# Performance work log

Hardware: AMD Instinct MI355X
Metric: run time of the kernel (lower is better)

Reference implementation:

```python
import jax, jax.numpy as jnp
import numpy as np
from jax import lax

WS = 8      # window size (square)
SS = 4      # shift size
HEADS = 8
K = 9       # snake-conv kernel size
CENTER = K // 2
EXT = 1.0   # extend_scope


def _shift_attn_mask(H, W):
    # static numpy construction of Swin shift mask -> [num_windows, L, L]
    m = np.zeros((H, W), dtype=np.float32)
    cnt = 0
    for hs in [(0, -WS), (-WS, -SS), (-SS, None)]:
        for ws_ in [(0, -WS), (-WS, -SS), (-SS, None)]:
            m[hs[0]:hs[1], ws_[0]:ws_[1]] = cnt
            cnt += 1
    m = m.reshape(H // WS, WS, W // WS, WS).transpose(0, 2, 1, 3).reshape(-1, WS * WS)
    d = m[:, None, :] - m[:, :, None]
    return jnp.asarray(np.where(d != 0, -100.0, 0.0).astype(np.float32))


def shifted_window_attention(x, qkv_w, qkv_b, proj_w, proj_b, rel_bias):
    B, H, W, C = x.shape
    d = C // HEADS
    x = jnp.roll(x, shift=(-SS, -SS), axis=(1, 2))
    nH, nW = H // WS, W // WS
    nwin, L = nH * nW, WS * WS
    # window partition -> [B*nwin, L, C]
    xw = x.reshape(B, nH, WS, nW, WS, C).transpose(0, 1, 3, 2, 4, 5).reshape(B * nwin, L, C)
    qkv = (xw @ qkv_w.T + qkv_b).reshape(B * nwin, L, 3, HEADS, d).transpose(2, 0, 3, 1, 4)
    q, k, v = qkv[0] * (d ** -0.5), qkv[1], qkv[2]
    attn = jnp.einsum('nhld,nhmd->nhlm', q, k) + rel_bias[None]
    amask = _shift_attn_mask(H, W)  # [nwin, L, L]
    attn = attn.reshape(B, nwin, HEADS, L, L) + amask[None, :, None]
    attn = jax.nn.softmax(attn.reshape(B * nwin, HEADS, L, L), axis=-1)
    out = jnp.einsum('nhlm,nhmd->nhld', attn, v).transpose(0, 2, 1, 3).reshape(B * nwin, L, C)
    out = out @ proj_w.T + proj_b
    out = out.reshape(B, nH, nW, WS, WS, C).transpose(0, 1, 3, 2, 4, 5).reshape(B, H, W, C)
    return jnp.roll(out, shift=(SS, SS), axis=(1, 2))


def snake_coordinate_map(offset):
    # offset [B, 2K, Wd, Hd], morph=0: cumulative y offsets from the kernel center
    B, _, Wd, Hd = offset.shape
    y_off = offset[:, :K]
    # y_new[center]=0; y_new[center+i]=sum_{j=1..i} y_off[center+j]; mirror below
    up = jnp.cumsum(y_off[:, CENTER + 1:], axis=1)
    down = jnp.cumsum(y_off[:, :CENTER][:, ::-1], axis=1)[:, ::-1]
    y_cum = jnp.concatenate([down, jnp.zeros((B, 1, Wd, Hd), offset.dtype), up], axis=1)
    y_center = jnp.arange(Wd, dtype=offset.dtype)[None, None, :, None]
    y_new = y_center + EXT * y_cum                              # [B,K,Wd,Hd]
    x_spread = jnp.linspace(-CENTER, CENTER, K, dtype=offset.dtype)[None, :, None, None]
    x_center = jnp.arange(Hd, dtype=offset.dtype)[None, None, None, :]
    x_new = jnp.broadcast_to(x_center + x_spread, (B, K, Wd, Hd))
    # rearrange 'b k w h -> b (w k) h'
    y_map = y_new.transpose(0, 2, 1, 3).reshape(B, Wd * K, Hd)
    x_map = x_new.transpose(0, 2, 1, 3).reshape(B, Wd * K, Hd)
    return y_map, x_map


def bilinear_sample(feat, ymap, xmap):
    Hin, Win = feat.shape[-2], feat.shape[-1]
    y = jnp.clip(ymap, 0.0, Hin - 1.0)
    x = jnp.clip(xmap, 0.0, Win - 1.0)
    y0f, x0f = jnp.floor(y), jnp.floor(x)
    wy, wx = y - y0f, x - x0f
    y0 = y0f.astype(jnp.int32); x0 = x0f.astype(jnp.int32)
    y1 = jnp.minimum(y0 + 1, Hin - 1); x1 = jnp.minimum(x0 + 1, Win - 1)
    g = jax.vmap(lambda f, yy, xx: f[:, yy, xx])  # -> [B,C,Ho,Wo]
    v00 = g(feat, y0, x0); v01 = g(feat, y0, x1)
    v10 = g(feat, y1, x0); v11 = g(feat, y1, x1)
    wy = wy[:, None]; wx = wx[:, None]
    return v00 * (1 - wy) * (1 - wx) + v01 * (1 - wy) * wx + v10 * wy * (1 - wx) + v11 * wy * wx


def _forward(x, qkv_weight, qkv_bias, proj_weight, proj_bias, rel_bias, offset, dsc_weight, dsc_bias):
    y = shifted_window_attention(x, qkv_weight, qkv_bias, proj_weight, proj_bias, rel_bias)
    feat = y.transpose(0, 3, 1, 2)                      # NCHW
    ymap, xmap = snake_coordinate_map(offset)
    samp = bilinear_sample(feat, ymap, xmap)            # [B,C,H*K,W]
    out = lax.conv_general_dilated(samp, dsc_weight, window_strides=(K, 1), padding='VALID',
                                   dimension_numbers=('NCHW', 'OIHW', 'NCHW'))
    return jax.nn.relu(out + dsc_bias[None, :, None, None])


def setup_inputs() -> dict:
    key = jax.random.key(0)
    ks = jax.random.split(key, 9)
    B, H, W, C = 8, 64, 64, 256
    return {
        'x': jax.random.normal(ks[0], (B, H, W, C), jnp.float32),
        'qkv_weight': jax.random.normal(ks[1], (3 * C, C), jnp.float32) * 0.05,
        'qkv_bias': jax.random.normal(ks[2], (3 * C,), jnp.float32) * 0.05,
        'proj_weight': jax.random.normal(ks[3], (C, C), jnp.float32) * 0.05,
        'proj_bias': jax.random.normal(ks[4], (C,), jnp.float32) * 0.05,
        'rel_bias': jax.random.normal(ks[5], (HEADS, WS * WS, WS * WS), jnp.float32) * 0.05,
        'offset': jax.random.normal(ks[6], (B, 2 * K, H, W), jnp.float32),
        'dsc_weight': jax.random.normal(ks[7], (C, C, K, 1), jnp.float32) * 0.02,
        'dsc_bias': jax.random.normal(ks[8], (C,), jnp.float32) * 0.02,
    }


def reference(x, qkv_weight, qkv_bias, proj_weight, proj_bias, rel_bias, offset, dsc_weight, dsc_bias):
    return _forward(x, qkv_weight, qkv_bias, proj_weight, proj_bias, rel_bias, offset, dsc_weight, dsc_bias)
```

## Files before the change

### kernel.cpp

```cpp
#include <hip/hip_runtime.h>
#include <math.h>


#define NFLOAT_BUF 8388608

typedef float f32x4 __attribute__((ext_vector_type(4)));
typedef __bf16 bf16x8 __attribute__((ext_vector_type(8)));
typedef _Float16 f16x8 __attribute__((ext_vector_type(8)));

__device__ inline unsigned pack2_bf16(float a, float b) {
    union { float f; unsigned u; } ua, ub;
    ua.f = a; ub.f = b;
    unsigned ra = (ua.u + 0x7FFFu + ((ua.u >> 16) & 1u)) >> 16;
    unsigned rb = (ub.u + 0x7FFFu + ((ub.u >> 16) & 1u)) & 0xFFFF0000u;
    return (ra & 0xFFFFu) | rb;
}

__global__ __launch_bounds__(256) void prep_kernel(
    const float* __restrict__ x, unsigned short* __restrict__ xb,
    const float* __restrict__ qkv_w, unsigned short* __restrict__ wb,
    const float* __restrict__ proj_w, _Float16* __restrict__ pwh,
    const float* __restrict__ dsc_w, _Float16* __restrict__ wT,
    const float* __restrict__ offset, float* __restrict__ ymap) {
    int bid = blockIdx.x, tid = threadIdx.x;
    if (bid < 4096) {
        int t = bid * 256 + tid;
        const float4* s = (const float4*)(x + (size_t)t * 8);
        float4 a = s[0], b = s[1];
        uint4 o;
        o.x = pack2_bf16(a.x, a.y); o.y = pack2_bf16(a.z, a.w);
        o.z = pack2_bf16(b.x, b.y); o.w = pack2_bf16(b.z, b.w);
        *(uint4*)(xb + (size_t)t * 8) = o;
    } else if (bid < 4192) {
        int t = (bid - 4096) * 256 + tid;
        if (t < 24576) {
            const float4* s = (const float4*)(qkv_w + (size_t)t * 8);
            float4 a = s[0], b = s[1];
            uint4 o;
            o.x = pack2_bf16(a.x, a.y); o.y = pack2_bf16(a.z, a.w);
            o.z = pack2_bf16(b.x, b.y); o.w = pack2_bf16(b.z, b.w);
            *(uint4*)(wb + (size_t)t * 8) = o;
        }
    } else if (bid < 4224) {
        int t = (bid - 4192) * 256 + tid;
        if (t < 8192) {
            const float4* s = (const float4*)(proj_w + (size_t)t * 8);
            float4 a = s[0], b = s[1];
            union { _Float16 h[8]; uint4 u; } o;
            o.h[0] = (_Float16)a.x; o.h[1] = (_Float16)a.y;
            o.h[2] = (_Float16)a.z; o.h[3] = (_Float16)a.w;
            o.h[4] = (_Float16)b.x; o.h[5] = (_Float16)b.y;
            o.h[6] = (_Float16)b.z; o.h[7] = (_Float16)b.w;
            *(uint4*)(pwh + (size_t)t * 8) = o.u;
        }
    } else if (bid < 6528) {
        int t = (bid - 4224) * 256 + tid;
        int o = t / 2304;
        int kk = t - o * 2304;
        int k = kk >> 8, i = kk & 255;
        wT[t] = (_Float16)dsc_w[(o * 256 + i) * 9 + k];
    } else {
        int t = (bid - 6528) * 256 + tid;
        int hd = t & 63;
        int wd = (t >> 6) & 63;
        int b  = t >> 12;
        const float* op = offset + ((size_t)(b * 18) * 64 + wd) * 64 + hd;
        float yo[9];
        #pragma unroll
        for (int k = 0; k < 9; ++k) yo[k] = op[(size_t)k * 4096];
        float cum[9];
        cum[4] = 0.0f;
        float s = 0.0f;
        for (int j = 3; j >= 0; --j) { s += yo[j]; cum[j] = s; }
        s = 0.0f;
        for (int j = 5; j < 9; ++j) { s += yo[j]; cum[j] = s; }
        float wdf = (float)wd;
        float* yp = ymap + ((size_t)(b * 576 + wd * 9)) * 64 + hd;
        #pragma unroll
        for (int k = 0; k < 9; ++k) yp[(size_t)k * 64] = wdf + cum[k];
    }
}

__global__ __launch_bounds__(256) void qkv_mfma_kernel(
    const unsigned short* __restrict__ xb, const unsigned short* __restrict__ wb,
    const float* __restrict__ qkv_b,
    _Float16* __restrict__ qh, _Float16* __restrict__ kh, _Float16* __restrict__ vt) {

    __shared__ __align__(16) char Asb[8192];
    __shared__ __align__(16) char Bsb[32768];
    __shared__ unsigned rowoff[64];

    int nb = blockIdx.x;
    int m0 = blockIdx.y * 64;
    int tid = threadIdx.x;
    int lane = tid & 63, w = tid >> 6;
    int gw = m0 >> 6;

    if (tid < 64) {
        int l = tid;
        int b = gw >> 6, win = gw & 63;
        int rh = ((win >> 3) << 3) + (l >> 3);
        int rw = ((win & 7) << 3) + (l & 7);
        int sh = (rh + 4) & 63, sw = (rw + 4) & 63;
        rowoff[l] = (unsigned)(((b * 64 + sh) * 64 + sw) * 512);
    }

    f32x4 acc[4][4];
    #pragma unroll
    for (int m = 0; m < 4; ++m)
        #pragma unroll
        for (int n = 0; n < 4; ++n) {
            f32x4 z = {0.0f, 0.0f, 0.0f, 0.0f};
            acc[m][n] = z;
        }

    const char* xc = (const char*)xb;
    const char* wc = (const char*)wb;
    int rA = (lane & 15) * 128;
    int u0 = (((lane >> 4)    ) ^ (lane & 7)) << 4;
    int u1 = ((4 + (lane >> 4)) ^ (lane & 7)) << 4;

    __syncthreads();

    for (int c = 0; c < 4; ++c) {
        #pragma unroll
        for (int r = 0; r < 2; ++r) {
            int pos = r * 256 + tid;
            int row = pos >> 3, u = pos & 7;
            const char* src = xc + rowoff[row] + c * 128 + ((u ^ (row & 7)) << 4);
            __builtin_amdgcn_global_load_lds(
                (const __attribute__((address_space(1))) unsigned int*)src,
                (__attribute__((address_space(3))) unsigned int*)(Asb + pos * 16),
                16, 0, 0);
        }
        #pragma unroll
        for (int r = 0; r < 8; ++r) {
            int pos = r * 256 + tid;
            int n = pos >> 3, u = pos & 7;
            const char* src = wc + (size_t)(nb * 256 + n) * 512 + c * 128 + ((u ^ (n & 7)) << 4);
            __builtin_amdgcn_global_load_lds(
                (const __attribute__((address_space(1))) unsigned int*)src,
                (__attribute__((address_space(3))) unsigned int*)(Bsb + pos * 16),
                16, 0, 0);
        }
        __syncthreads();

        bf16x8 av[4][2], bv[4][2];
        #pragma unroll
        for (int m = 0; m < 4; ++m) {
            av[m][0] = *(const bf16x8*)(Asb + m * 2048 + rA + u0);
            av[m][1] = *(const bf16x8*)(Asb + m * 2048 + rA + u1);
        }
        #pragma unroll
        for (int n = 0; n < 4; ++n) {
            bv[n][0] = *(const bf16x8*)(Bsb + w * 8192 + n * 2048 + rA + u0);
            bv[n][1] = *(const bf16x8*)(Bsb + w * 8192 + n * 2048 + rA + u1);
        }
        #pragma unroll
        for (int m = 0; m < 4; ++m)
            #pragma unroll
            for (int n = 0; n < 4; ++n) {
                acc[m][n] = __builtin_amdgcn_mfma_f32_16x16x32_bf16(av[m][0], bv[n][0], acc[m][n], 0, 0, 0);
                acc[m][n] = __builtin_amdgcn_mfma_f32_16x16x32_bf16(av[m][1], bv[n][1], acc[m][n], 0, 0, 0);
            }
        __syncthreads();
    }

    float scale = (nb == 0) ? 0.17677669529663689f : 1.0f;
    #pragma unroll
    for (int nf = 0; nf < 4; ++nf) {
        int o = w * 64 + nf * 16 + (lane & 15);
        float bias = qkv_b[nb * 256 + o];
        int hh = o >> 5, dd = o & 31;
        if (nb < 2) {
            _Float16* dstb = (nb == 0) ? qh : kh;
            _Float16* base = dstb + ((size_t)(gw * 8 + hh) * 64) * 32 + dd;
            #pragma unroll
            for (int mf = 0; mf < 4; ++mf) {
                int l0 = mf * 16 + (lane >> 4) * 4;
                #pragma unroll
                for (int j = 0; j < 4; ++j)
                    base[(size_t)(l0 + j) * 32] = (_Float16)((acc[mf][nf][j] + bias) * scale);
            }
        } else {
            _Float16* base = vt + ((size_t)(gw * 8 + hh) * 32 + dd) * 64;
            #pragma unroll
            for (int mf = 0; mf < 4; ++mf) {
                int l0 = mf * 16 + (lane >> 4) * 4;
                union { _Float16 x[4]; uint2 u; } pk;
                #pragma unroll
                for (int j = 0; j < 4; ++j) pk.x[j] = (_Float16)(acc[mf][nf][j] + bias);
                *(uint2*)(base + l0) = pk.u;
            }
        }
    }
}

__global__ __launch_bounds__(512, 4) void attn_proj_kernel(
    const _Float16* __restrict__ qh, const _Float16* __restrict__ kh,
    const _Float16* __restrict__ vt, const float* __restrict__ rel_bias,
    const _Float16* __restrict__ pwh, const float* __restrict__ proj_b,
    _Float16* __restrict__ feath) {

    __shared__ __align__(16) char SH[65536];
    int n = blockIdx.x;
    int win = n & 63;
    int wy = win >> 3, wx = win & 7;
    int tid = threadIdx.x, lane = tid & 63, h = tid >> 6;
    int qc = lane & 15, g = lane >> 4;
    char* P = SH + h * 8192;

    const _Float16* qp = qh + (size_t)(n * 8 + h) * 2048;
    const _Float16* kp = kh + (size_t)(n * 8 + h) * 2048;
    const _Float16* vp = vt + (size_t)(n * 8 + h) * 2048;
    const float* rb = rel_bias + (size_t)h * 4096;

    int rk[16];
    #pragma unroll
    for (int mt = 0; mt < 4; ++mt)
        #pragma unroll
        for (int j = 0; j < 4; ++j) {
            int key = mt * 16 + g * 4 + j;
            int rh = wy * 8 + (key >> 3), rw = wx * 8 + (key & 7);
            rk[mt * 4 + j] = (rh < 56 ? 0 : (rh < 60 ? 1 : 2)) * 3
                           + (rw < 56 ? 0 : (rw < 60 ? 1 : 2));
        }

    f16x8 kf[4];
    #pragma unroll
    for (int mt = 0; mt < 4; ++mt)
        kf[mt] = *(const f16x8*)(kp + (mt * 16 + qc) * 32 + g * 8);

    #pragma unroll
    for (int nt = 0; nt < 4; ++nt) {
        int q = nt * 16 + qc;
        int rqh = wy * 8 + (q >> 3), rqw = wx * 8 + (q & 7);
        int rq = (rqh < 56 ? 0 : (rqh < 60 ? 1 : 2)) * 3
               + (rqw < 56 ? 0 : (rqw < 60 ? 1 : 2));
        f16x8 qf = *(const f16x8*)(qp + q * 32 + g * 8);

        f32x4 s[4];
        #pragma unroll
        for (int mt = 0; mt < 4; ++mt) {
            f32x4 z = {0.0f, 0.0f, 0.0f, 0.0f};
            s[mt] = __builtin_amdgcn_mfma_f32_16x16x32_f16(kf[mt], qf, z, 0, 0, 0);
        }

        float vals[16];
        #pragma unroll
        for (int mt = 0; mt < 4; ++mt) {
            float4 bv4 = *(const float4*)(rb + q * 64 + mt * 16 + g * 4);
            vals[mt * 4 + 0] = s[mt][0] + bv4.x + (rk[mt * 4 + 0] != rq ? -100.0f : 0.0f);
            vals[mt * 4 + 1] = s[mt][1] + bv4.y + (rk[mt * 4 + 1] != rq ? -100.0f : 0.0f);
            vals[mt * 4 + 2] = s[mt][2] + bv4.z + (rk[mt * 4 + 2] != rq ? -100.0f : 0.0f);
            vals[mt * 4 + 3] = s[mt][3] + bv4.w + (rk[mt * 4 + 3] != rq ? -100.0f : 0.0f);
        }

        float mx = vals[0];
        #pragma unroll
        for (int i = 1; i < 16; ++i) mx = fmaxf(mx, vals[i]);
        mx = fmaxf(mx, __shfl_xor(mx, 16));
        mx = fmaxf(mx, __shfl_xor(mx, 32));

        float sum = 0.0f;
        #pragma unroll
        for (int i = 0; i < 16; ++i) { vals[i] = __expf(vals[i] - mx); sum += vals[i]; }
        sum += __shfl_xor(sum, 16);
        sum += __shfl_xor(sum, 32);
        float inv = 1.0f / sum;

        #pragma unroll
        for (int mt = 0; mt < 4; ++mt) {
            union { _Float16 x[4]; uint2 u; } pk4;
            #pragma unroll
            for (int j = 0; j < 4; ++j) pk4.x[j] = (_Float16)(vals[mt * 4 + j] * inv);
            int off = (mt * 32 + g * 8) ^ ((q & 7) << 4);
            *(uint2*)(P + q * 128 + off) = pk4.u;
        }
    }

    f16x8 pa[4][2];
    #pragma unroll
    for (int im = 0; im < 4; ++im)
        #pragma unroll
        for (int ks = 0; ks < 2; ++ks) {
            int row = im * 16 + qc;
            int off = (ks * 64 + g * 16) ^ ((row & 7) << 4);
            pa[im][ks] = *(const f16x8*)(P + row * 128 + off);
        }
    f16x8 bvv[2][2];
    #pragma unroll
    for (int in = 0; in < 2; ++in)
        #pragma unroll
        for (int ks = 0; ks < 2; ++ks)
            bvv[in][ks] = *(const f16x8*)(vp + (in * 16 + qc) * 64 + ks * 32 + g * 8);

    f32x4 acc[4][2];
    #pragma unroll
    for (int im = 0; im < 4; ++im)
        #pragma unroll
        for (int in = 0; in < 2; ++in) {
            f32x4 z = {0.0f, 0.0f, 0.0f, 0.0f};
            acc[im][in] = z;
        }
    #pragma unroll
    for (int im = 0; im < 4; ++im)
        #pragma unroll
        for (int in = 0; in < 2; ++in) {
            acc[im][in] = __builtin_amdgcn_mfma_f32_16x16x32_f16(pa[im][0], bvv[in][0], acc[im][in], 0, 0, 0);
            acc[im][in] = __builtin_amdgcn_mfma_f32_16x16x32_f16(pa[im][1], bvv[in][1], acc[im][in], 0, 0, 0);
        }

    __syncthreads();

    char* aob = SH;
    char* Bsb = SH + 32768;
    #pragma unroll
    for (int im = 0; im < 4; ++im)
        #pragma unroll
        for (int in = 0; in < 2; ++in)
            #pragma unroll
            for (int j = 0; j < 4; ++j) {
                int row = im * 16 + g * 4 + j;
                int f = h * 32 + in * 16 + qc;
                *(_Float16*)(aob + row * 512 + ((((f >> 3) ^ (row & 7)) << 4) + (f & 7) * 2)) =
                    (_Float16)acc[im][in][j];
            }
    __syncthreads();

    int w04 = h & 3, wm = h >> 2;
    const char* wcp = (const char*)pwh;
    int bidx = n >> 6;

    f32x4 pacc[2][4];
    #pragma unroll
    for (int m = 0; m < 2; ++m)
        #pragma unroll
        for (int nn = 0; nn < 4; ++nn) {
            f32x4 z = {0.0f, 0.0f, 0.0f, 0.0f};
            pacc[m][nn] = z;
        }

    for (int c = 0; c < 4; ++c) {
        #pragma unroll
        for (int r = 0; r < 4; ++r) {
            int pos = r * 512 + tid;
            int nr = pos >> 3, uu = pos & 7;
            const char* src = wcp + (size_t)nr * 512 + c * 128 + ((uu ^ (nr & 7)) << 4);
            __builtin_amdgcn_global_load_lds(
                (const __attribute__((address_space(1))) unsigned int*)src,
                (__attribute__((address_space(3))) unsigned int*)(Bsb + pos * 16),
                16, 0, 0);
        }
        __syncthreads();

        f16x8 av2[2][2], bv2[4][2];
        #pragma unroll
        for (int m = 0; m < 2; ++m) {
            int row = wm * 32 + m * 16 + qc;
            #pragma unroll
            for (int ks = 0; ks < 2; ++ks) {
                int u = c * 8 + ks * 4 + g;
                av2[m][ks] = *(const f16x8*)(aob + row * 512 + ((u ^ (row & 7)) << 4));
            }
        }
        #pragma unroll
        for (int nn = 0; nn < 4; ++nn) {
            int oc = w04 * 64 + nn * 16 + qc;
            #pragma unroll
            for (int ks = 0; ks < 2; ++ks)
                bv2[nn][ks] = *(const f16x8*)(Bsb + oc * 128 + (((ks * 4 + g) ^ (oc & 7)) << 4));
        }
        #pragma unroll
        for (int m = 0; m < 2; ++m)
            #pragma unroll
            for (int nn = 0; nn < 4; ++nn) {
                pacc[m][nn] = __builtin_amdgcn_mfma_f32_16x16x32_f16(av2[m][0], bv2[nn][0], pacc[m][nn], 0, 0, 0);
                pacc[m][nn] = __builtin_amdgcn_mfma_f32_16x16x32_f16(av2[m][1], bv2[nn][1], pacc[m][nn], 0, 0, 0);
            }
        __syncthreads();
    }

    #pragma unroll
    for (int nn = 0; nn < 4; ++nn) {
        int f = w04 * 64 + nn * 16 + qc;
        float bias = proj_b[f];
        #pragma unroll
        for (int m = 0; m < 2; ++m) {
            #pragma unroll
            for (int j = 0; j < 4; ++j) {
                int px = wm * 32 + m * 16 + g * 4 + j;
                int rh = ((win >> 3) << 3) + (px >> 3);
                int rw = ((win & 7) << 3) + (px & 7);
                int p = (rh + 4) & 63;
                int qq = (rw + 4) & 63;
                feath[((size_t)(bidx * 64 + p) * 64 + qq) * 256 + f] =
                    (_Float16)(pacc[m][nn][j] + bias);
            }
        }
    }
}

__global__ __launch_bounds__(512) void sample_conv_mfma4_kernel(
    const _Float16* __restrict__ feath, const float* __restrict__ ymap,
    const _Float16* __restrict__ wT2h, const float* __restrict__ dsc_b,
    float* __restrict__ out) {

    __shared__ __align__(16) char Ab[2][16384];
    __shared__ __align__(16) char Bb[2][32768];
    __shared__ unsigned row0[2][9][64];
    __shared__ unsigned row1[2][9][64];
    __shared__ float    wyv[2][9][64];

    int blk = blockIdx.x;
    int b = blk & 7, wd0 = (blk >> 3) * 2;
    int tid = threadIdx.x;
    int lane = tid & 63, w = tid >> 6;
    int qc = lane & 15, g = lane >> 4;
    int ph = w >> 2, nq = w & 3;

    for (int idx = tid; idx < 1152; idx += 512) {
        int wdl = idx / 576;
        int r = idx - wdl * 576;
        int k = r >> 6, hd = r & 63;
        int wd = wd0 + wdl;
        float y = ymap[((size_t)(b * 576 + wd * 9 + k)) * 64 + hd];
        y = fminf(fmaxf(y, 0.0f), 63.0f);
        float y0f = floorf(y);
        int y0 = (int)y0f;
        int y1 = min(y0 + 1, 63);
        int xc = min(max(hd + k - 4, 0), 63);
        row0[wdl][k][hd] = (unsigned)(((b * 64 + y0) * 64 + xc) * 512);
        row1[wdl][k][hd] = (unsigned)(((b * 64 + y1) * 64 + xc) * 512);
        wyv[wdl][k][hd] = y - y0f;
    }

    f32x4 acc[4][4];
    #pragma unroll
    for (int m = 0; m < 4; ++m)
        #pragma unroll
        for (int n = 0; n < 4; ++n) {
            f32x4 z = {0.0f, 0.0f, 0.0f, 0.0f};
            acc[m][n] = z;
        }

    const char* featc = (const char*)feath;
    const char* wc    = (const char*)wT2h;

    int pxA[2], sAv[2];
    #pragma unroll
    for (int r = 0; r < 2; ++r) {
        int pos = r * 512 + tid;
        pxA[r] = pos >> 3;
        sAv[r] = pos & 7;
    }

    int rAa = qc * 128;
    int u0 = ((g    ) ^ (qc & 7)) << 4;
    int u1 = ((4 + g) ^ (qc & 7)) << 4;

    __syncthreads();

    #pragma unroll
    for (int r = 0; r < 4; ++r) {
        int pos = r * 512 + tid;
        int n = pos >> 3, uu = pos & 7;
        const char* src = wc + n * 4608 + 0 * 128 + ((uu ^ (n & 7)) << 4);
        __builtin_amdgcn_global_load_lds(
            (const __attribute__((address_space(1))) unsigned int*)src,
            (__attribute__((address_space(3))) unsigned int*)(Bb[0] + pos * 16),
            16, 0, 0);
    }
    #pragma unroll
    for (int r = 0; r < 2; ++r) {
        int px = pxA[r], sA = sAv[r];
        int wdl = px >> 6, hd = px & 63;
        unsigned b0 = row0[wdl][0][hd] + sA * 16;
        unsigned b1 = row1[wdl][0][hd] + sA * 16;
        float wy = wyv[wdl][0][hd];
        f16x8 v0 = *(const f16x8*)(featc + b0);
        f16x8 v1 = *(const f16x8*)(featc + b1);
        _Float16 wyh = (_Float16)wy;
        _Float16 omh = (_Float16)(1.0f - wy);
        f16x8 res = v0 * omh + v1 * wyh;
        *(f16x8*)(Ab[0] + px * 128 + ((sA ^ (px & 7)) << 4)) = res;
    }
    __syncthreads();

    for (int c = 0; c < 36; ++c) {
        int cur = c & 1, nxt = cur ^ 1;

        f16x8 s0[2], s1[2];
        float swy[2];
        if (c < 35) {
            int cn = c + 1;
            int ks = cn >> 2, cib = (cn & 3) * 128;
            #pragma unroll
            for (int r = 0; r < 4; ++r) {
                int pos = r * 512 + tid;
                int n = pos >> 3, uu = pos & 7;
                const char* src = wc + n * 4608 + cn * 128 + ((uu ^ (n & 7)) << 4);
                __builtin_amdgcn_global_load_lds(
                    (const __attribute__((address_space(1))) unsigned int*)src,
                    (__attribute__((address_space(3))) unsigned int*)(Bb[nxt] + pos * 16),
                    16, 0, 0);
            }
            #pragma unroll
            for (int r = 0; r < 2; ++r) {
                int px = pxA[r], sA = sAv[r];
                int wdl = px >> 6, hd = px & 63;
                unsigned b0 = row0[wdl][ks][hd] + cib + sA * 16;
                unsigned b1 = row1[wdl][ks][hd] + cib + sA * 16;
                swy[r] = wyv[wdl][ks][hd];
                s0[r] = *(const f16x8*)(featc + b0);
                s1[r] = *(const f16x8*)(featc + b1);
            }
        }

        f16x8 av[4][2], bv[4][2];
        #pragma unroll
        for (int m = 0; m < 4; ++m) {
            char* abase = Ab[cur] + ph * 8192 + m * 2048 + rAa;
            av[m][0] = *(const f16x8*)(abase + u0);
            av[m][1] = *(const f16x8*)(abase + u1);
        }
        #pragma unroll
        for (int n = 0; n < 4; ++n) {
            char* bbase = Bb[cur] + nq * 8192 + n * 2048 + rAa;
            bv[n][0] = *(const f16x8*)(bbase + u0);
            bv[n][1] = *(const f16x8*)(bbase + u1);
        }
        #pragma unroll
        for (int m = 0; m < 4; ++m)
            #pragma unroll
            for (int n = 0; n < 4; ++n) {
                acc[m][n] = __builtin_amdgcn_mfma_f32_16x16x32_f16(av[m][0], bv[n][0], acc[m][n], 0, 0, 0);
                acc[m][n] = __builtin_amdgcn_mfma_f32_16x16x32_f16(av[m][1], bv[n][1], acc[m][n], 0, 0, 0);
            }

        if (c < 35) {
            #pragma unroll
            for (int r = 0; r < 2; ++r) {
                int px = pxA[r], sA = sAv[r];
                _Float16 wyh = (_Float16)swy[r];
                _Float16 omh = (_Float16)(1.0f - swy[r]);
                f16x8 res = s0[r] * omh + s1[r] * wyh;
                *(f16x8*)(Ab[nxt] + px * 128 + ((sA ^ (px & 7)) << 4)) = res;
            }
        }
        __syncthreads();
    }

    #pragma unroll
    for (int n = 0; n < 4; ++n) {
        int o = nq * 64 + n * 16 + qc;
        float bvs = dsc_b[o];
        float* orow = out + ((size_t)(b * 256 + o) * 64 + (wd0 + ph)) * 64;
        #pragma unroll
        for (int m = 0; m < 4; ++m) {
            int px = m * 16 + g * 4;
            float4 res;
            res.x = fmaxf(acc[m][n][0] + bvs, 0.0f);
            res.y = fmaxf(acc[m][n][1] + bvs, 0.0f);
            res.z = fmaxf(acc[m][n][2] + bvs, 0.0f);
            res.w = fmaxf(acc[m][n][3] + bvs, 0.0f);
            *(float4*)(orow + px) = res;
        }
    }
}

extern "C" void kernel_launch(void* const* d_in, const int* in_sizes, int n_in,
                              void* d_out, int out_size, void* d_ws, size_t ws_size,
                              hipStream_t stream) {
    (void)in_sizes; (void)n_in; (void)out_size; (void)ws_size;
    const float* x        = (const float*)d_in[0];
    const float* qkv_w    = (const float*)d_in[1];
    const float* qkv_b    = (const float*)d_in[2];
    const float* proj_w   = (const float*)d_in[3];
    const float* proj_b   = (const float*)d_in[4];
    const float* rel_bias = (const float*)d_in[5];
    const float* offset   = (const float*)d_in[6];
    const float* dsc_w    = (const float*)d_in[7];
    const float* dsc_b    = (const float*)d_in[8];
    float* out = (float*)d_out;

    unsigned short* wsu = (unsigned short*)d_ws;
    _Float16* qh = (_Float16*)wsu;
    _Float16* kh = (_Float16*)(wsu + NFLOAT_BUF);
    _Float16* vt = (_Float16*)(wsu + 2 * (size_t)NFLOAT_BUF);
    _Float16* feath = (_Float16*)(wsu + 3 * (size_t)NFLOAT_BUF);
    unsigned short* xb      = wsu + 4 * (size_t)NFLOAT_BUF;
    unsigned short* wb      = wsu + 5 * (size_t)NFLOAT_BUF;
    _Float16* pwh           = (_Float16*)(wb + 196608);
    _Float16* wT2h          = (_Float16*)((unsigned short*)pwh + 65536);
    float* ymap = (float*)((unsigned short*)wT2h + 589824);

    prep_kernel<<<6656, 256, 0, stream>>>(x, xb, qkv_w, wb, proj_w, pwh,
                                          dsc_w, wT2h, offset, ymap);
    qkv_mfma_kernel<<<dim3(3, 512), 256, 0, stream>>>(xb, wb, qkv_b, qh, kh, vt);
    attn_proj_kernel<<<512, 512, 0, stream>>>(qh, kh, vt, rel_bias, pwh, proj_b, feath);
    sample_conv_mfma4_kernel<<<256, 512, 0, stream>>>(feath, ymap, wT2h, dsc_b, out);
}
```

Before: 204.7 us.

## Double-buffer QKV GEMM tiles, enlarge M tile, stage Q/K stores through LDS

The QKV projection kernel now uses 512-thread blocks, each computing a 128-row by 256-column tile. The K-chunk loads go into double-buffered LDS so the global-to-LDS copy of the next chunk overlaps the MFMA work on the current one. Q and K outputs, which were written as scattered 2-byte stores, are transposed through a swizzled LDS buffer and written out as 16-byte vector stores. The cost is much more LDS per block (about 97 KB), which limits occupancy, and half as many blocks in the grid.

```diff
diff --git a/kernel.cpp b/kernel.cpp
--- a/kernel.cpp
+++ b/kernel.cpp
@@ -81,28 +81,33 @@
     }
 }
 
-__global__ __launch_bounds__(256) void qkv_mfma_kernel(
+__global__ __launch_bounds__(512, 2) void qkv_mfma2_kernel(
     const unsigned short* __restrict__ xb, const unsigned short* __restrict__ wb,
     const float* __restrict__ qkv_b,
     _Float16* __restrict__ qh, _Float16* __restrict__ kh, _Float16* __restrict__ vt) {
 
-    __shared__ __align__(16) char Asb[8192];
-    __shared__ __align__(16) char Bsb[32768];
-    __shared__ unsigned rowoff[64];
+    __shared__ __align__(16) char SH[98816];
+    char* Ab[2] = { SH, SH + 16384 };
+    char* Bb[2] = { SH + 32768, SH + 65536 };
+    unsigned* rowoff = (unsigned*)(SH + 98304);
 
     int nb = blockIdx.x;
-    int m0 = blockIdx.y * 64;
+    int m0 = blockIdx.y * 128;
+    int gw0 = m0 >> 6;
     int tid = threadIdx.x;
     int lane = tid & 63, w = tid >> 6;
-    int gw = m0 >> 6;
-
-    if (tid < 64) {
+    int qc = lane & 15, g = lane >> 4;
+    int ph = w >> 2, nq = w & 3;
+
+    if (tid < 128) {
         int l = tid;
+        int gw = gw0 + (l >> 6);
         int b = gw >> 6, win = gw & 63;
-        int rh = ((win >> 3) << 3) + (l >> 3);
-        int rw = ((win & 7) << 3) + (l & 7);
-        int sh = (rh + 4) & 63, sw = (rw + 4) & 63;
-        rowoff[l] = (unsigned)(((b * 64 + sh) * 64 + sw) * 512);
+        int l2 = l & 63;
+        int rh = ((win >> 3) << 3) + (l2 >> 3);
+        int rw = ((win & 7) << 3) + (l2 & 7);
+        int sh_ = (rh + 4) & 63, sw_ = (rw + 4) & 63;
+        rowoff[l] = (unsigned)(((b * 64 + sh_) * 64 + sw_) * 512);
     }
 
     f32x4 acc[4][4];
@@ -116,45 +121,73 @@
 
     const char* xc = (const char*)xb;
     const char* wc = (const char*)wb;
-    int rA = (lane & 15) * 128;
-    int u0 = (((lane >> 4)    ) ^ (lane & 7)) << 4;
-    int u1 = ((4 + (lane >> 4)) ^ (lane & 7)) << 4;
+    int rAa = qc * 128;
+    int u0 = ((g    ) ^ (qc & 7)) << 4;
+    int u1 = ((4 + g) ^ (qc & 7)) << 4;
 
     __syncthreads();
 
+    #pragma unroll
+    for (int r = 0; r < 2; ++r) {
+        int pos = r * 512 + tid;
+        int row = pos >> 3, u = pos & 7;
+        const char* src = xc + rowoff[row] + ((u ^ (row & 7)) << 4);
+        __builtin_amdgcn_global_load_lds(
+            (const __attribute__((address_space(1))) unsigned int*)src,
+            (__attribute__((address_space(3))) unsigned int*)(Ab[0] + pos * 16),
+            16, 0, 0);
+    }
+    #pragma unroll
+    for (int r = 0; r < 4; ++r) {
+        int pos = r * 512 + tid;
+        int n = pos >> 3, u = pos & 7;
+        const char* src = wc + (size_t)(nb * 256 + n) * 512 + ((u ^ (n & 7)) << 4);
+        __builtin_amdgcn_global_load_lds(
+            (const __attribute__((address_space(1))) unsigned int*)src,
+            (__attribute__((address_space(3))) unsigned int*)(Bb[0] + pos * 16),
+            16, 0, 0);
+    }
+    __syncthreads();
+
     for (int c = 0; c < 4; ++c) {
-        #pragma unroll
-        for (int r = 0; r < 2; ++r) {
-            int pos = r * 256 + tid;
-            int row = pos >> 3, u = pos & 7;
-            const char* src = xc + rowoff[row] + c * 128 + ((u ^ (row & 7)) << 4);
-            __builtin_amdgcn_global_load_lds(
-                (const __attribute__((address_space(1))) unsigned int*)src,
-                (__attribute__((address_space(3))) unsigned int*)(Asb + pos * 16),
-                16, 0, 0);
-        }
-        #pragma unroll
-        for (int r = 0; r < 8; ++r) {
-            int pos = r * 256 + tid;
-            int n = pos >> 3, u = pos & 7;
-            const char* src = wc + (size_t)(nb * 256 + n) * 512 + c * 128 + ((u ^ (n & 7)) << 4);
-            __builtin_amdgcn_global_load_lds(
-                (const __attribute__((address_space(1))) unsigned int*)src,
-                (__attribute__((address_space(3))) unsigned int*)(Bsb + pos * 16),
-                16, 0, 0);
-        }
-        __syncthreads();
+        int cur = c & 1, nxt = cur ^ 1;
+
+        if (c < 3) {
+            int cn = c + 1;
+            #pragma unroll
+            for (int r = 0; r < 2; ++r) {
+                int pos = r * 512 + tid;
+                int row = pos >> 3, u = pos & 7;
+                const char* src = xc + rowoff[row] + cn * 128 + ((u ^ (row & 7)) << 4);
+                __builtin_amdgcn_global_load_lds(
+                    (const __attribute__((address_space(1))) unsigned int*)src,
+                    (__attribute__((address_space(3))) unsigned int*)(Ab[nxt] + pos * 16),
+                    16, 0, 0);
+            }
+            #pragma unroll
+            for (int r = 0; r < 4; ++r) {
+                int pos = r * 512 + tid;
+                int n = pos >> 3, u = pos & 7;
+                const char* src = wc + (size_t)(nb * 256 + n) * 512 + cn * 128 + ((u ^ (n & 7)) << 4);
+                __builtin_amdgcn_global_load_lds(
+                    (const __attribute__((address_space(1))) unsigned int*)src,
+                    (__attribute__((address_space(3))) unsigned int*)(Bb[nxt] + pos * 16),
+                    16, 0, 0);
+            }
+        }
 
         bf16x8 av[4][2], bv[4][2];
         #pragma unroll
         for (int m = 0; m < 4; ++m) {
-            av[m][0] = *(const bf16x8*)(Asb + m * 2048 + rA + u0);
-            av[m][1] = *(const bf16x8*)(Asb + m * 2048 + rA + u1);
+            char* abase = Ab[cur] + ph * 8192 + m * 2048 + rAa;
+            av[m][0] = *(const bf16x8*)(abase + u0);
+            av[m][1] = *(const bf16x8*)(abase + u1);
         }
         #pragma unroll
         for (int n = 0; n < 4; ++n) {
-            bv[n][0] = *(const bf16x8*)(Bsb + w * 8192 + n * 2048 + rA + u0);
-            bv[n][1] = *(const bf16x8*)(Bsb + w * 8192 + n * 2048 + rA + u1);
+            char* bbase = Bb[cur] + nq * 8192 + n * 2048 + rAa;
+            bv[n][0] = *(const bf16x8*)(bbase + u0);
+            bv[n][1] = *(const bf16x8*)(bbase + u1);
         }
         #pragma unroll
         for (int m = 0; m < 4; ++m)
@@ -166,32 +199,48 @@
         __syncthreads();
     }
 
-    float scale = (nb == 0) ? 0.17677669529663689f : 1.0f;
-    #pragma unroll
-    for (int nf = 0; nf < 4; ++nf) {
-        int o = w * 64 + nf * 16 + (lane & 15);
-        float bias = qkv_b[nb * 256 + o];
-        int hh = o >> 5, dd = o & 31;
-        if (nb < 2) {
-            _Float16* dstb = (nb == 0) ? qh : kh;
-            _Float16* base = dstb + ((size_t)(gw * 8 + hh) * 64) * 32 + dd;
-            #pragma unroll
-            for (int mf = 0; mf < 4; ++mf) {
-                int l0 = mf * 16 + (lane >> 4) * 4;
-                #pragma unroll
-                for (int j = 0; j < 4; ++j)
-                    base[(size_t)(l0 + j) * 32] = (_Float16)((acc[mf][nf][j] + bias) * scale);
-            }
-        } else {
-            _Float16* base = vt + ((size_t)(gw * 8 + hh) * 32 + dd) * 64;
-            #pragma unroll
-            for (int mf = 0; mf < 4; ++mf) {
-                int l0 = mf * 16 + (lane >> 4) * 4;
+    if (nb == 2) {
+        #pragma unroll
+        for (int n = 0; n < 4; ++n) {
+            int o = nq * 64 + n * 16 + qc;
+            float bias = qkv_b[512 + o];
+            int hh = o >> 5, dd = o & 31;
+            _Float16* base = vt + ((size_t)((gw0 + ph) * 8 + hh) * 32 + dd) * 64;
+            #pragma unroll
+            for (int m = 0; m < 4; ++m) {
+                int l0 = m * 16 + g * 4;
                 union { _Float16 x[4]; uint2 u; } pk;
                 #pragma unroll
-                for (int j = 0; j < 4; ++j) pk.x[j] = (_Float16)(acc[mf][nf][j] + bias);
+                for (int j = 0; j < 4; ++j) pk.x[j] = (_Float16)(acc[m][n][j] + bias);
                 *(uint2*)(base + l0) = pk.u;
             }
+        }
+    } else {
+        float scale = (nb == 0) ? 0.17677669529663689f : 1.0f;
+        char* eL = SH + 32768;
+        #pragma unroll
+        for (int n = 0; n < 4; ++n) {
+            int f = nq * 64 + n * 16 + qc;
+            float bias = qkv_b[nb * 256 + f];
+            int slot = f >> 3, fin = (f & 7) * 2;
+            #pragma unroll
+            for (int m = 0; m < 4; ++m)
+                #pragma unroll
+                for (int j = 0; j < 4; ++j) {
+                    int l = ph * 64 + m * 16 + g * 4 + j;
+                    *(_Float16*)(eL + l * 512 + ((slot ^ (l & 7)) << 4) + fin) =
+                        (_Float16)((acc[m][n][j] + bias) * scale);
+                }
+        }
+        __syncthreads();
+        _Float16* dstb = (nb == 0) ? qh : kh;
+        #pragma unroll
+        for (int r = 0; r < 8; ++r) {
+            int s = r * 512 + tid;
+            int h = s >> 9, l = (s >> 2) & 127, p = s & 3;
+            uint4 vdat = *(const uint4*)(eL + l * 512 + (((h * 4 + p) ^ (l & 7)) << 4));
+            int gw = gw0 + (l >> 6);
+            *(uint4*)(dstb + ((size_t)(gw * 8 + h) * 64 + (l & 63)) * 32 + p * 8) = vdat;
         }
     }
 }
@@ -597,7 +646,7 @@
 
     prep_kernel<<<6656, 256, 0, stream>>>(x, xb, qkv_w, wb, proj_w, pwh,
                                           dsc_w, wT2h, offset, ymap);
-    qkv_mfma_kernel<<<dim3(3, 512), 256, 0, stream>>>(xb, wb, qkv_b, qh, kh, vt);
+    qkv_mfma2_kernel<<<dim3(3, 256), 512, 0, stream>>>(xb, wb, qkv_b, qh, kh, vt);
     attn_proj_kernel<<<512, 512, 0, stream>>>(qh, kh, vt, rel_bias, pwh, proj_b, feath);
     sample_conv_mfma4_kernel<<<256, 512, 0, stream>>>(feath, ymap, wT2h, dsc_b, out);
 }
```

Measured after the change: 208.2 us. About the same (+1.7%).
